# Performance work log

Measured on AMD Instinct MI355X. Metric: run time of the kernel, lower is better.

Reference implementation:

```python
import jax, jax.numpy as jnp
import numpy as np

EPS = 1e-7   # GENConv message eps
LN_EPS = 1e-5


def _ln(x, g, b):
    mu = jnp.mean(x, axis=-1, keepdims=True)
    var = jnp.mean((x - mu) ** 2, axis=-1, keepdims=True)
    return (x - mu) * jax.lax.rsqrt(var + LN_EPS) * g + b


def _genconv(h, e, src, dst, W1, b1, g1, bt1, W2, b2, t):
    # GENConv with softmax aggregation and 2-layer MLP (Linear->LN->ReLU->Linear)
    N = h.shape[0]
    m = jax.nn.relu(h[src] + e) + EPS                  # [E,H] messages
    logit = m * t
    mx = jax.ops.segment_max(logit, dst, num_segments=N)   # per-dst, per-channel max
    ex = jnp.exp(logit - mx[dst])
    den = jax.ops.segment_sum(ex, dst, num_segments=N)
    alpha = ex / jnp.maximum(den[dst], 1e-16)          # per-dst softmax weights
    agg = jax.ops.segment_sum(m * alpha, dst, num_segments=N)
    z = agg + h                                        # out + x_r
    z = jnp.dot(z, W1.T) + b1                          # [N,2H]
    z = jax.nn.relu(_ln(z, g1, bt1))
    return jnp.dot(z, W2.T) + b2                       # [N,H]


def setup_inputs() -> dict:
    key = jax.random.key(0)
    ks = jax.random.split(key, 10)
    B, S, H, L, deg = 16, 4096, 64, 4, 16
    N = B * S
    E = N * deg  # 65536 edges per sample, repeated structure
    x = jax.random.normal(ks[0], (N,), jnp.float32)
    edge_index = jax.random.randint(ks[1], (2, E), 0, N)
    edge_attr = jax.random.normal(ks[2], (E,), jnp.float32)
    batch = jnp.repeat(jnp.arange(B, dtype=jnp.int32), S)

    def nrm(k, shape, fan_in):
        return jax.random.normal(k, shape, jnp.float32) / np.float32(np.sqrt(fan_in))

    return dict(
        x=x, edge_index=edge_index, edge_attr=edge_attr, batch=batch, input_size=S,
        node_W=nrm(ks[3], (H, 1), 1), node_b=jnp.zeros((H,), jnp.float32),
        edge_W=nrm(ks[4], (H, 1), 1), edge_b=jnp.zeros((H,), jnp.float32),
        conv_W1=nrm(ks[5], (L, 2 * H, H), H), conv_b1=jnp.zeros((L, 2 * H), jnp.float32),
        conv_lng=jnp.ones((L, 2 * H), jnp.float32), conv_lnb=jnp.zeros((L, 2 * H), jnp.float32),
        conv_W2=nrm(ks[6], (L, H, 2 * H), 2 * H), conv_b2=jnp.zeros((L, H), jnp.float32),
        conv_t=jnp.ones((L,), jnp.float32),
        ln_g=jnp.ones((L, H), jnp.float32), ln_b=jnp.zeros((L, H), jnp.float32),
        lin_W=nrm(ks[7], (1, S * H), S * H), lin_b=jnp.zeros((1,), jnp.float32),
    )


def reference(x, edge_index, edge_attr, batch, input_size,
              node_W, node_b, edge_W, edge_b,
              conv_W1, conv_b1, conv_lng, conv_lnb, conv_W2, conv_b2, conv_t,
              ln_g, ln_b, lin_W, lin_b):
    N = x.shape[0]
    B = N // input_size
    src, dst = edge_index[0], edge_index[1]
    # node encoder: Linear(1,H) applied to every scalar node feature (batched GEMV)
    h = x[:, None] * node_W[:, 0][None, :] + node_b    # [N,H]
    # edge encoder: only row 0 of reshaped edge_attr is encoded, then repeated B times
    ea0 = edge_attr.reshape(B, -1)[0]                  # [E/B]
    eenc = ea0[:, None] * edge_W[:, 0][None, :] + edge_b
    e = jnp.tile(eenc, (B, 1))                         # [E,H]
    L = conv_W1.shape[0]
    # layer 0: conv only
    h = _genconv(h, e, src, dst, conv_W1[0], conv_b1[0], conv_lng[0], conv_lnb[0],
                 conv_W2[0], conv_b2[0], conv_t[0])
    # layers 1..L-1: res+ blocks (norm -> relu -> [dropout disabled, eval] -> conv -> residual)
    for l in range(1, L):
        hh = jax.nn.relu(_ln(h, ln_g[l], ln_b[l]))
        hh = _genconv(hh, e, src, dst, conv_W1[l], conv_b1[l], conv_lng[l], conv_lnb[l],
                      conv_W2[l], conv_b2[l], conv_t[l])
        h = h + hh
    h = jax.nn.relu(_ln(h, ln_g[0], ln_b[0]))
    # per-sample flatten + Linear readout (batch ids are contiguous blocks)
    y = h.reshape(B, -1) @ lin_W.T + lin_b             # [B,1]
    return y.reshape(-1)                               # [B]
```

## Files before the change

kernel.cpp:

```cpp
#include <hip/hip_runtime.h>

namespace {

typedef __attribute__((ext_vector_type(8))) short bf16x8;
typedef __attribute__((ext_vector_type(4))) float f32x4;

constexpr int NN = 65536;
constexpr int NE = 1 << 20;
constexpr int H2 = 128;
constexpr int NL = 4;
constexpr float GEPS = 1e-7f;
constexpr float LNEPS = 1e-5f;
constexpr float LOG2E = 1.44269504088896340736f;

__device__ inline unsigned f2bf(float f) {
  unsigned u = __builtin_bit_cast(unsigned, f);
  return (u + 0x7fffu + ((u >> 16) & 1u)) >> 16;
}
__device__ inline float bf2f(unsigned b) {
  unsigned u = b << 16;
  return __builtin_bit_cast(float, u);
}

__global__ __launch_bounds__(256) void kA0(const int* __restrict__ dst,
                                           int* __restrict__ bcnt) {
  __shared__ int h[256];
  int t = threadIdx.x;
  h[t] = 0;
  __syncthreads();
  int bs = blockIdx.x * 4096;
#pragma unroll 4
  for (int i = 0; i < 16; ++i) {
    int d = dst[bs + i * 256 + t];
    atomicAdd(&h[d >> 8], 1);
  }
  __syncthreads();
  atomicAdd(&bcnt[t], h[t]);
}

__global__ __launch_bounds__(256) void kScanB(const int* __restrict__ bcnt,
                                              int* __restrict__ bbase,
                                              int* __restrict__ cursorA) {
  __shared__ int s[256];
  int t = threadIdx.x;
  int v = bcnt[t];
  s[t] = v;
  __syncthreads();
  for (int dd = 1; dd < 256; dd <<= 1) {
    int val = (t >= dd) ? s[t - dd] : 0;
    __syncthreads();
    s[t] += val;
    __syncthreads();
  }
  int ex = s[t] - v;
  bbase[t] = ex;
  cursorA[t] = ex;
  if (t == 255) bbase[256] = NE;
}

__global__ __launch_bounds__(256) void kA1(const int* __restrict__ src,
                                           const int* __restrict__ dst,
                                           const float* __restrict__ ea0,
                                           int* __restrict__ cursorA,
                                           uint2* __restrict__ binned) {
  __shared__ int h[256], lcur[256], base[256];
  int t = threadIdx.x;
  h[t] = 0;
  lcur[t] = 0;
  __syncthreads();
  int bs = blockIdx.x * 4096;
#pragma unroll 4
  for (int i = 0; i < 16; ++i) {
    int d = dst[bs + i * 256 + t];
    atomicAdd(&h[d >> 8], 1);
  }
  __syncthreads();
  base[t] = atomicAdd(&cursorA[t], h[t]);
  __syncthreads();
  for (int i = 0; i < 16; ++i) {
    int e = bs + i * 256 + t;
    int d = dst[e];
    int s = src[e];
    float a = ea0[e & 65535];
    int b = d >> 8;
    int k = atomicAdd(&lcur[b], 1);
    uint2 r;
    r.x = (unsigned)s | ((unsigned)(d & 255) << 16);
    r.y = __builtin_bit_cast(unsigned, a);
    binned[base[b] + k] = r;
  }
}

__global__ __launch_bounds__(256) void kB(const uint2* __restrict__ binned,
                                          const int* __restrict__ bbase,
                                          uint2* __restrict__ recs,
                                          int* __restrict__ offsets) {
  __shared__ int h[256], sc[256], ex[256], lcur[256];
  int t = threadIdx.x;
  int b = blockIdx.x;
  int s0 = bbase[b], s1 = bbase[b + 1], n = s1 - s0;
  h[t] = 0;
  lcur[t] = 0;
  __syncthreads();
  for (int i = t; i < n; i += 256) atomicAdd(&h[(binned[s0 + i].x >> 16) & 255], 1);
  __syncthreads();
  sc[t] = h[t];
  __syncthreads();
  for (int dd = 1; dd < 256; dd <<= 1) {
    int val = (t >= dd) ? sc[t - dd] : 0;
    __syncthreads();
    sc[t] += val;
    __syncthreads();
  }
  ex[t] = sc[t] - h[t];
  offsets[b * 256 + t] = s0 + ex[t];
  if (b == 0 && t == 0) offsets[NN] = NE;
  __syncthreads();
  for (int i = t; i < n; i += 256) {
    uint2 r = binned[s0 + i];
    int d8 = (r.x >> 16) & 255;
    int k = atomicAdd(&lcur[d8], 1);
    uint2 o;
    o.x = r.x & 0xffffu;
    o.y = r.y;
    recs[s0 + ex[d8] + k] = o;
  }
}

template <int L0>
__global__ __launch_bounds__(256) void k_agg(const unsigned short* __restrict__ hinb,
                                             const float* __restrict__ hinf,
                                             const float* __restrict__ x,
                                             const float* __restrict__ nW,
                                             const float* __restrict__ nb,
                                             const float* __restrict__ eW,
                                             const float* __restrict__ eb,
                                             const int* __restrict__ offsets,
                                             const uint2* __restrict__ recs,
                                             const float* __restrict__ conv_t, int layer,
                                             float* __restrict__ zbuf) {
  int lane = threadIdx.x & 63;
  int d = blockIdx.x * 4 + (threadIdx.x >> 6);
  float t2 = conv_t[layer] * LOG2E;
  float eWl = eW[lane], ebl = eb[lane];
  float nWl = 0.f, nbl = 0.f;
  if (L0) { nWl = nW[lane]; nbl = nb[lane]; }
  int off = __builtin_amdgcn_readfirstlane(offsets[d]);
  int end = __builtin_amdgcn_readfirstlane(offsets[d + 1]);
  int n = end - off;
  float hself = L0 ? fmaf(x[d], nWl, nbl) : hinf[d * 64 + lane];
  const uint2* rp = recs + off;

  float den0 = 0.f, num0 = 0.f, den1 = 0.f, num1 = 0.f;
  int k = 0;
  for (; k + 8 <= n; k += 8) {
    float m[8];
#pragma unroll
    for (int j = 0; j < 8; ++j) {
      uint2 r = rp[k + j];
      int s = __builtin_amdgcn_readfirstlane((int)r.x);
      float a = __builtin_bit_cast(float, __builtin_amdgcn_readfirstlane((int)r.y));
      float hs = L0 ? fmaf(x[s], nWl, nbl) : bf2f(hinb[(s << 6) + lane]);
      m[j] = fmaxf(fmaf(a, eWl, ebl) + hs, 0.f);
    }
    float e[8];
#pragma unroll
    for (int j = 0; j < 8; ++j) e[j] = exp2f(m[j] * t2);
    den0 += (e[0] + e[1]) + (e[2] + e[3]);
    den1 += (e[4] + e[5]) + (e[6] + e[7]);
    num0 += fmaf(m[0], e[0], m[1] * e[1]) + fmaf(m[2], e[2], m[3] * e[3]);
    num1 += fmaf(m[4], e[4], m[5] * e[5]) + fmaf(m[6], e[6], m[7] * e[7]);
  }
  for (; k < n; ++k) {
    uint2 r = rp[k];
    int s = __builtin_amdgcn_readfirstlane((int)r.x);
    float a = __builtin_bit_cast(float, __builtin_amdgcn_readfirstlane((int)r.y));
    float hs = L0 ? fmaf(x[s], nWl, nbl) : bf2f(hinb[(s << 6) + lane]);
    float m = fmaxf(fmaf(a, eWl, ebl) + hs, 0.f);
    float e = exp2f(m * t2);
    den0 += e;
    num0 = fmaf(m, e, num0);
  }
  float den = den0 + den1, num = num0 + num1;
  float agg = num / fmaxf(den, 1e-16f) + GEPS;
  zbuf[d * 64 + lane] = agg + hself;
}

__global__ __launch_bounds__(256) void k_wprep(const float* __restrict__ W1,
                                               const float* __restrict__ W2,
                                               unsigned short* __restrict__ w1hi,
                                               unsigned short* __restrict__ w1lo,
                                               unsigned short* __restrict__ w2hi,
                                               unsigned short* __restrict__ w2lo) {
  int t = blockIdx.x * 256 + threadIdx.x;
  int which = t >> 15;
  int o = t & 32767;
  int l = o >> 13, idx = o & 8191;
  int fid = idx >> 9, lane = (idx >> 3) & 63, j = idx & 7;
  int lr = lane & 15, lg = lane >> 4;
  if (which == 0) {
    int nt = fid >> 1, ks = fid & 1;
    int m = nt * 16 + lr, k = ks * 32 + lg * 8 + j;
    float v = W1[l * 8192 + m * 64 + k];
    unsigned hi = f2bf(v);
    w1hi[o] = (unsigned short)hi;
    w1lo[o] = (unsigned short)f2bf(v - bf2f(hi));
  } else {
    int mt = fid >> 2, ks = fid & 3;
    int m = mt * 16 + lr, k = ks * 32 + lg * 8 + j;
    float v = W2[l * 8192 + m * 128 + k];
    unsigned hi = f2bf(v);
    w2hi[o] = (unsigned short)hi;
    w2lo[o] = (unsigned short)f2bf(v - bf2f(hi));
  }
}

__global__ __launch_bounds__(256) void k_mlpmm(const float* __restrict__ zbuf,
                                               float* __restrict__ h,
                                               float* __restrict__ hinf,
                                               unsigned short* __restrict__ hinb,
                                               const unsigned short* __restrict__ w1hi,
                                               const unsigned short* __restrict__ w1lo,
                                               const unsigned short* __restrict__ w2hi,
                                               const unsigned short* __restrict__ w2lo,
                                               const float* __restrict__ b1,
                                               const float* __restrict__ g1,
                                               const float* __restrict__ bt1,
                                               const float* __restrict__ b2,
                                               const float* __restrict__ gnx,
                                               const float* __restrict__ bnx,
                                               const float* __restrict__ linW,
                                               float* __restrict__ partials,
                                               int mode) {
  __shared__ unsigned Yb[4][16 * 132];
  int tid = threadIdx.x, wv = tid >> 6, l = tid & 63;
  int lr = l & 15, lg = l >> 4;
  unsigned* Y = Yb[wv];
  int n0 = (blockIdx.x * 4 + wv) * 16;

  bf16x8 zh[2], zl[2];
#pragma unroll
  for (int ks = 0; ks < 2; ++ks) {
    const float* zp = zbuf + (n0 + lr) * 64 + ks * 32 + lg * 8;
    float4 a = *(const float4*)zp, b = *(const float4*)(zp + 4);
    float zv[8] = {a.x, a.y, a.z, a.w, b.x, b.y, b.z, b.w};
    bf16x8 hh, ll;
#pragma unroll
    for (int j = 0; j < 8; ++j) {
      unsigned hi = f2bf(zv[j]);
      hh[j] = (short)hi;
      ll[j] = (short)f2bf(zv[j] - bf2f(hi));
    }
    zh[ks] = hh;
    zl[ks] = ll;
  }

  f32x4 C1[8];
#pragma unroll
  for (int nt = 0; nt < 8; ++nt) {
    bf16x8 a0h = *(const bf16x8*)(w1hi + ((nt * 2 + 0) * 64 + l) * 8);
    bf16x8 a0l = *(const bf16x8*)(w1lo + ((nt * 2 + 0) * 64 + l) * 8);
    bf16x8 a1h = *(const bf16x8*)(w1hi + ((nt * 2 + 1) * 64 + l) * 8);
    bf16x8 a1l = *(const bf16x8*)(w1lo + ((nt * 2 + 1) * 64 + l) * 8);
    f32x4 c = {0.f, 0.f, 0.f, 0.f};
    c = __builtin_amdgcn_mfma_f32_16x16x32_bf16(a0h, zh[0], c, 0, 0, 0);
    c = __builtin_amdgcn_mfma_f32_16x16x32_bf16(a0l, zh[0], c, 0, 0, 0);
    c = __builtin_amdgcn_mfma_f32_16x16x32_bf16(a0h, zl[0], c, 0, 0, 0);
    c = __builtin_amdgcn_mfma_f32_16x16x32_bf16(a1h, zh[1], c, 0, 0, 0);
    c = __builtin_amdgcn_mfma_f32_16x16x32_bf16(a1l, zh[1], c, 0, 0, 0);
    c = __builtin_amdgcn_mfma_f32_16x16x32_bf16(a1h, zl[1], c, 0, 0, 0);
    C1[nt] = c;
  }

  float s = 0.f, q = 0.f;
#pragma unroll
  for (int nt = 0; nt < 8; ++nt) {
    float4 bv = *(const float4*)(b1 + nt * 16 + lg * 4);
#pragma unroll
    for (int r = 0; r < 4; ++r) {
      float v = C1[nt][r] + ((const float*)&bv)[r];
      C1[nt][r] = v;
      s += v;
      q += v * v;
    }
  }
  s += __shfl_xor(s, 16); q += __shfl_xor(q, 16);
  s += __shfl_xor(s, 32); q += __shfl_xor(q, 32);
  float mu = s * (1.f / 128.f);
  float rs = rsqrtf(q * (1.f / 128.f) - mu * mu + LNEPS);
#pragma unroll
  for (int nt = 0; nt < 8; ++nt) {
    float4 gv = *(const float4*)(g1 + nt * 16 + lg * 4);
    float4 btv = *(const float4*)(bt1 + nt * 16 + lg * 4);
    unsigned pk[4];
#pragma unroll
    for (int r = 0; r < 4; ++r) {
      float y = fmaxf((C1[nt][r] - mu) * rs * ((const float*)&gv)[r] + ((const float*)&btv)[r], 0.f);
      unsigned hi = f2bf(y);
      unsigned lo = f2bf(y - bf2f(hi));
      pk[r] = hi | (lo << 16);
    }
    int idx = lr * 132 + ((nt * 16 + lg * 4) ^ ((lr & 7) << 2));
    *(uint4*)(Y + idx) = make_uint4(pk[0], pk[1], pk[2], pk[3]);
  }

  bf16x8 yh[4], yl[4];
#pragma unroll
  for (int ks = 0; ks < 4; ++ks) {
    bf16x8 hh, ll;
#pragma unroll
    for (int half = 0; half < 2; ++half) {
      int cb = ks * 32 + lg * 8 + half * 4;
      uint4 v = *(const uint4*)(Y + lr * 132 + (cb ^ ((lr & 7) << 2)));
      unsigned dw[4] = {v.x, v.y, v.z, v.w};
#pragma unroll
      for (int j = 0; j < 4; ++j) {
        hh[half * 4 + j] = (short)(dw[j] & 0xffffu);
        ll[half * 4 + j] = (short)(dw[j] >> 16);
      }
    }
    yh[ks] = hh;
    yl[ks] = ll;
  }

  f32x4 C2[4];
#pragma unroll
  for (int mt = 0; mt < 4; ++mt) {
    f32x4 c = {0.f, 0.f, 0.f, 0.f};
#pragma unroll
    for (int ks = 0; ks < 4; ++ks) {
      bf16x8 ah = *(const bf16x8*)(w2hi + ((mt * 4 + ks) * 64 + l) * 8);
      bf16x8 al = *(const bf16x8*)(w2lo + ((mt * 4 + ks) * 64 + l) * 8);
      c = __builtin_amdgcn_mfma_f32_16x16x32_bf16(ah, yh[ks], c, 0, 0, 0);
      c = __builtin_amdgcn_mfma_f32_16x16x32_bf16(al, yh[ks], c, 0, 0, 0);
      c = __builtin_amdgcn_mfma_f32_16x16x32_bf16(ah, yl[ks], c, 0, 0, 0);
    }
    C2[mt] = c;
  }

  int gnode = n0 + lr;
  float s2 = 0.f, q2 = 0.f;
#pragma unroll
  for (int mt = 0; mt < 4; ++mt) {
    float4 b2v = *(const float4*)(b2 + mt * 16 + lg * 4);
    float4 hr = {0.f, 0.f, 0.f, 0.f};
    if (mode != 0) hr = *(const float4*)(h + gnode * 64 + mt * 16 + lg * 4);
    float4 hv;
#pragma unroll
    for (int r = 0; r < 4; ++r) {
      float o = C2[mt][r] + ((const float*)&b2v)[r];
      float v = (mode == 0) ? o : ((const float*)&hr)[r] + o;
      ((float*)&hv)[r] = v;
      s2 += v;
      q2 += v * v;
      C2[mt][r] = v;
    }
    if (mode != 2) *(float4*)(h + gnode * 64 + mt * 16 + lg * 4) = hv;
  }
  s2 += __shfl_xor(s2, 16); q2 += __shfl_xor(q2, 16);
  s2 += __shfl_xor(s2, 32); q2 += __shfl_xor(q2, 32);
  float mu2 = s2 * (1.f / 64.f);
  float rs2 = rsqrtf(q2 * (1.f / 64.f) - mu2 * mu2 + LNEPS);
  if (mode != 2) {
#pragma unroll
    for (int mt = 0; mt < 4; ++mt) {
      float4 gv = *(const float4*)(gnx + mt * 16 + lg * 4);
      float4 bv = *(const float4*)(bnx + mt * 16 + lg * 4);
      float4 fo;
#pragma unroll
      for (int r = 0; r < 4; ++r)
        ((float*)&fo)[r] = fmaxf((C2[mt][r] - mu2) * rs2 * ((const float*)&gv)[r] + ((const float*)&bv)[r], 0.f);
      *(float4*)(hinf + gnode * 64 + mt * 16 + lg * 4) = fo;
      uint2 pb;
      pb.x = f2bf(fo.x) | (f2bf(fo.y) << 16);
      pb.y = f2bf(fo.z) | (f2bf(fo.w) << 16);
      *(uint2*)(hinb + gnode * 64 + mt * 16 + lg * 4) = pb;
    }
  } else {
    float p = 0.f;
#pragma unroll
    for (int mt = 0; mt < 4; ++mt) {
      float4 gv = *(const float4*)(gnx + mt * 16 + lg * 4);
      float4 bv = *(const float4*)(bnx + mt * 16 + lg * 4);
      float4 lw = *(const float4*)(linW + (gnode & 4095) * 64 + mt * 16 + lg * 4);
#pragma unroll
      for (int r = 0; r < 4; ++r) {
        float f = fmaxf((C2[mt][r] - mu2) * rs2 * ((const float*)&gv)[r] + ((const float*)&bv)[r], 0.f);
        p += f * ((const float*)&lw)[r];
      }
    }
    p += __shfl_xor(p, 16);
    p += __shfl_xor(p, 32);
    if (lg == 0) partials[gnode] = p;
  }
}

__global__ __launch_bounds__(256) void k_readout2(const float* __restrict__ partials,
                                                  const float* __restrict__ linb,
                                                  float* __restrict__ out) {
  __shared__ float s[256];
  int b = blockIdx.x, t = threadIdx.x;
  float acc = 0.0f;
  for (int i = t; i < 4096; i += 256) acc += partials[b * 4096 + i];
  s[t] = acc;
  __syncthreads();
  for (int d = 128; d > 0; d >>= 1) {
    if (t < d) s[t] += s[t + d];
    __syncthreads();
  }
  if (t == 0) out[b] = s[0] + linb[0];
}

}

extern "C" void kernel_launch(void* const* d_in, const int* in_sizes, int n_in,
                              void* d_out, int out_size, void* d_ws, size_t ws_size,
                              hipStream_t stream) {
  const float* x = (const float*)d_in[0];
  const int* ei = (const int*)d_in[1];
  const float* ea = (const float*)d_in[2];
  const float* nW = (const float*)d_in[5];
  const float* nb = (const float*)d_in[6];
  const float* eW = (const float*)d_in[7];
  const float* eb = (const float*)d_in[8];
  const float* W1 = (const float*)d_in[9];
  const float* b1 = (const float*)d_in[10];
  const float* g1 = (const float*)d_in[11];
  const float* bt1 = (const float*)d_in[12];
  const float* W2 = (const float*)d_in[13];
  const float* b2 = (const float*)d_in[14];
  const float* ct = (const float*)d_in[15];
  const float* lng = (const float*)d_in[16];
  const float* lnb = (const float*)d_in[17];
  const float* linW = (const float*)d_in[18];
  const float* linb = (const float*)d_in[19];
  float* out = (float*)d_out;

  const int* src = ei;
  const int* dst = ei + NE;

  char* p = (char*)d_ws;
  auto alloc = [&](size_t bytes) {
    char* r = p;
    p += (bytes + 255) & ~size_t(255);
    return r;
  };
  float* h = (float*)alloc(size_t(NN) * 64 * 4);
  float* hinf = (float*)alloc(size_t(NN) * 64 * 4);
  unsigned short* hinb = (unsigned short*)alloc(size_t(NN) * 64 * 2);
  float* zbuf = (float*)alloc(size_t(NN) * 64 * 4);
  uint2* binned = (uint2*)alloc(size_t(NE) * 8);
  uint2* recs = (uint2*)alloc(size_t(NE) * 8);
  int* offsets = (int*)alloc(size_t(NN + 1) * 4);
  int* bcnt = (int*)alloc(256 * 4);
  int* bbase = (int*)alloc(257 * 4);
  int* cursorA = (int*)alloc(256 * 4);
  float* partials = (float*)alloc(size_t(NN) * 4);
  unsigned short* w1hi = (unsigned short*)alloc(4 * 8192 * 2);
  unsigned short* w1lo = (unsigned short*)alloc(4 * 8192 * 2);
  unsigned short* w2hi = (unsigned short*)alloc(4 * 8192 * 2);
  unsigned short* w2lo = (unsigned short*)alloc(4 * 8192 * 2);

  k_wprep<<<256, 256, 0, stream>>>(W1, W2, w1hi, w1lo, w2hi, w2lo);

  hipMemsetAsync(bcnt, 0, 256 * 4, stream);
  kA0<<<256, 256, 0, stream>>>(dst, bcnt);
  kScanB<<<1, 256, 0, stream>>>(bcnt, bbase, cursorA);
  kA1<<<256, 256, 0, stream>>>(src, dst, ea, cursorA, binned);
  kB<<<256, 256, 0, stream>>>(binned, bbase, recs, offsets);

  for (int l = 0; l < NL; ++l) {
    if (l == 0)
      k_agg<1><<<NN / 4, 256, 0, stream>>>(hinb, hinf, x, nW, nb, eW, eb,
                                           offsets, recs, ct, l, zbuf);
    else
      k_agg<0><<<NN / 4, 256, 0, stream>>>(hinb, hinf, x, nW, nb, eW, eb,
                                           offsets, recs, ct, l, zbuf);
    int mode = (l == 0) ? 0 : (l == NL - 1 ? 2 : 1);
    const float* gnext = (l == NL - 1) ? lng : lng + (l + 1) * 64;
    const float* bnext = (l == NL - 1) ? lnb : lnb + (l + 1) * 64;
    k_mlpmm<<<NN / 64, 256, 0, stream>>>(zbuf, h, hinf, hinb,
                                         w1hi + l * 8192, w1lo + l * 8192,
                                         w2hi + l * 8192, w2lo + l * 8192,
                                         b1 + l * H2, g1 + l * H2, bt1 + l * H2,
                                         b2 + l * 64, gnext, bnext,
                                         linW, partials, mode);
  }

  k_readout2<<<16, 256, 0, stream>>>(partials, linb, out);
}
```

Before: 310.9 us.

## Process four destination nodes per wave in aggregation via segmented reduction

Measured after the change: 526.1 us. 69.2% more time.

```diff
diff --git a/kernel.cpp b/kernel.cpp
--- a/kernel.cpp
+++ b/kernel.cpp
@@ -121,7 +121,7 @@
     int d8 = (r.x >> 16) & 255;
     int k = atomicAdd(&lcur[d8], 1);
     uint2 o;
-    o.x = r.x & 0xffffu;
+    o.x = (r.x & 0xffffu) | ((unsigned)(b * 256 + d8) << 16);
     o.y = r.y;
     recs[s0 + ex[d8] + k] = o;
   }
@@ -140,50 +140,88 @@
                                              const float* __restrict__ conv_t, int layer,
                                              float* __restrict__ zbuf) {
   int lane = threadIdx.x & 63;
-  int d = blockIdx.x * 4 + (threadIdx.x >> 6);
+  int wv = threadIdx.x >> 6;
+  int d0 = (blockIdx.x * 4 + wv) * 4;
   float t2 = conv_t[layer] * LOG2E;
   float eWl = eW[lane], ebl = eb[lane];
   float nWl = 0.f, nbl = 0.f;
   if (L0) { nWl = nW[lane]; nbl = nb[lane]; }
-  int off = __builtin_amdgcn_readfirstlane(offsets[d]);
-  int end = __builtin_amdgcn_readfirstlane(offsets[d + 1]);
+  int off = __builtin_amdgcn_readfirstlane(offsets[d0]);
+  int end = __builtin_amdgcn_readfirstlane(offsets[d0 + 4]);
   int n = end - off;
-  float hself = L0 ? fmaf(x[d], nWl, nbl) : hinf[d * 64 + lane];
   const uint2* rp = recs + off;
 
-  float den0 = 0.f, num0 = 0.f, den1 = 0.f, num1 = 0.f;
+  float hs0 = L0 ? fmaf(x[d0 + 0], nWl, nbl) : hinf[(d0 + 0) * 64 + lane];
+  float hs1 = L0 ? fmaf(x[d0 + 1], nWl, nbl) : hinf[(d0 + 1) * 64 + lane];
+  float hs2 = L0 ? fmaf(x[d0 + 2], nWl, nbl) : hinf[(d0 + 2) * 64 + lane];
+  float hs3 = L0 ? fmaf(x[d0 + 3], nWl, nbl) : hinf[(d0 + 3) * 64 + lane];
+  zbuf[(d0 + 0) * 64 + lane] = hs0 + GEPS;
+  zbuf[(d0 + 1) * 64 + lane] = hs1 + GEPS;
+  zbuf[(d0 + 2) * 64 + lane] = hs2 + GEPS;
+  zbuf[(d0 + 3) * 64 + lane] = hs3 + GEPS;
+
+  int curd = -1;
+  float den = 0.f, num = 0.f;
+
+  auto flush = [&]() {
+    if (curd >= 0) {
+      float agg = num / fmaxf(den, 1e-16f) + GEPS;
+      int ci = curd - d0;
+      float hsel = (ci == 0) ? hs0 : (ci == 1) ? hs1 : (ci == 2) ? hs2 : hs3;
+      zbuf[curd * 64 + lane] = agg + hsel;
+    }
+  };
+
   int k = 0;
   for (; k + 8 <= n; k += 8) {
     float m[8];
+    int dd[8];
 #pragma unroll
     for (int j = 0; j < 8; ++j) {
       uint2 r = rp[k + j];
-      int s = __builtin_amdgcn_readfirstlane((int)r.x);
+      unsigned rx = (unsigned)__builtin_amdgcn_readfirstlane((int)r.x);
       float a = __builtin_bit_cast(float, __builtin_amdgcn_readfirstlane((int)r.y));
+      int s = (int)(rx & 0xffffu);
+      dd[j] = (int)(rx >> 16);
       float hs = L0 ? fmaf(x[s], nWl, nbl) : bf2f(hinb[(s << 6) + lane]);
       m[j] = fmaxf(fmaf(a, eWl, ebl) + hs, 0.f);
     }
     float e[8];
 #pragma unroll
     for (int j = 0; j < 8; ++j) e[j] = exp2f(m[j] * t2);
-    den0 += (e[0] + e[1]) + (e[2] + e[3]);
-    den1 += (e[4] + e[5]) + (e[6] + e[7]);
-    num0 += fmaf(m[0], e[0], m[1] * e[1]) + fmaf(m[2], e[2], m[3] * e[3]);
-    num1 += fmaf(m[4], e[4], m[5] * e[5]) + fmaf(m[6], e[6], m[7] * e[7]);
+#pragma unroll
+    for (int j = 0; j < 8; ++j) {
+      if (dd[j] != curd) {
+        flush();
+        curd = dd[j];
+        den = e[j];
+        num = m[j] * e[j];
+      } else {
+        den += e[j];
+        num = fmaf(m[j], e[j], num);
+      }
+    }
   }
   for (; k < n; ++k) {
     uint2 r = rp[k];
-    int s = __builtin_amdgcn_readfirstlane((int)r.x);
+    unsigned rx = (unsigned)__builtin_amdgcn_readfirstlane((int)r.x);
     float a = __builtin_bit_cast(float, __builtin_amdgcn_readfirstlane((int)r.y));
+    int s = (int)(rx & 0xffffu);
+    int dj = (int)(rx >> 16);
     float hs = L0 ? fmaf(x[s], nWl, nbl) : bf2f(hinb[(s << 6) + lane]);
     float m = fmaxf(fmaf(a, eWl, ebl) + hs, 0.f);
     float e = exp2f(m * t2);
-    den0 += e;
-    num0 = fmaf(m, e, num0);
-  }
-  float den = den0 + den1, num = num0 + num1;
-  float agg = num / fmaxf(den, 1e-16f) + GEPS;
-  zbuf[d * 64 + lane] = agg + hself;
+    if (dj != curd) {
+      flush();
+      curd = dj;
+      den = e;
+      num = m * e;
+    } else {
+      den += e;
+      num = fmaf(m, e, num);
+    }
+  }
+  flush();
 }
 
 __global__ __launch_bounds__(256) void k_wprep(const float* __restrict__ W1,
@@ -471,11 +509,11 @@
 
   for (int l = 0; l < NL; ++l) {
     if (l == 0)
-      k_agg<1><<<NN / 4, 256, 0, stream>>>(hinb, hinf, x, nW, nb, eW, eb,
-                                           offsets, recs, ct, l, zbuf);
+      k_agg<1><<<NN / 16, 256, 0, stream>>>(hinb, hinf, x, nW, nb, eW, eb,
+                                            offsets, recs, ct, l, zbuf);
     else
-      k_agg<0><<<NN / 4, 256, 0, stream>>>(hinb, hinf, x, nW, nb, eW, eb,
-                                           offsets, recs, ct, l, zbuf);
+      k_agg<0><<<NN / 16, 256, 0, stream>>>(hinb, hinf, x, nW, nb, eW, eb,
+                                            offsets, recs, ct, l, zbuf);
     int mode = (l == 0) ? 0 : (l == NL - 1 ? 2 : 1);
     const float* gnext = (l == NL - 1) ? lng : lng + (l + 1) * 64;
     const float* bnext = (l == NL - 1) ? lnb : lnb + (l + 1) * 64;
```
